# Optimization experiments

Hardware: AMD Instinct MI355X
Metric: run time of the kernel (lower is better)

The kernel has to match this reference:

```python
import jax, jax.numpy as jnp
import numpy as np

B, T, D, H = 64, 512, 512, 128

def swish(x):
    return x * jax.nn.sigmoid(x)

def setup_inputs() -> dict:
    key = jax.random.key(0)
    ks = jax.random.split(key, 8)
    X = jax.random.normal(ks[0], (B, T, D), dtype=jnp.float32)
    # strictly-upper-triangular random binary adjacency -> valid DAG
    adj = jax.random.bernoulli(ks[1], 0.3, (T, T)).astype(jnp.float32)
    dag = jnp.triu(adj, k=1)
    s = 1.0 / np.sqrt(D)
    Wk = jax.random.normal(ks[2], (H, D), dtype=jnp.float32) * s
    bk = jax.random.normal(ks[3], (H,), dtype=jnp.float32) * 0.01
    Wq = jax.random.normal(ks[4], (H, D), dtype=jnp.float32) * s
    bq = jax.random.normal(ks[5], (H,), dtype=jnp.float32) * 0.01
    Wv = jax.random.normal(ks[6], (H, D), dtype=jnp.float32) * s
    bv = jax.random.normal(ks[7], (H,), dtype=jnp.float32) * 0.01
    return {"X": X, "dag": dag, "Wk": Wk, "bk": bk, "Wq": Wq, "bq": bq, "Wv": Wv, "bv": bv}

def reference(X, dag, Wk, bk, Wq, bq, Wv, bv):
    K = swish(jnp.einsum('btd,hd->bth', X, Wk) + bk)  # [B,T,H]
    Q = swish(jnp.einsum('btd,hd->bth', X, Wq) + bq)
    V = swish(jnp.einsum('btd,hd->bth', X, Wv) + bv)
    S_qk = jnp.einsum('bqh,bkh->bqk', Q, K) / jnp.sqrt(jnp.float32(H))  # [B,T,T]
    dagT = dag.T  # [T,T]
    Sprime = dagT * jnp.einsum('ij,bjk->bik', dagT, S_qk)  # [B,T,T]
    # masked_fill(Sprime == 0, -inf) then softmax; rows that are all -inf
    # would produce NaN in torch and are replaced by zeros -> do it nan-free.
    nz = Sprime != 0
    masked = jnp.where(nz, Sprime, -jnp.inf)
    row_valid = jnp.any(nz, axis=-1, keepdims=True)  # [B,T,1]
    masked_safe = jnp.where(row_valid, masked, 0.0)
    probs = jax.nn.softmax(masked_safe, axis=-1) * row_valid  # [B,T,T]
    Vprime = jnp.einsum('ij,bjh->bih', dagT, V)  # [B,T,H]
    O = jnp.einsum('bqk,bkh->bqh', probs, V) + Vprime
    return O
```

## Files before the change

kernel.cpp:

```cpp
#include <hip/hip_runtime.h>
#include <hip/hip_bf16.h>

#define Bn 64
#define Tn 512
#define Dn 512
#define Hn 128
#define BT (Bn*Tn)

typedef unsigned short u16;
typedef unsigned long long u64;
typedef __attribute__((ext_vector_type(8))) short bf16x8;
typedef __attribute__((ext_vector_type(4))) float f32x4;

__device__ __forceinline__ u16 f2bf(float f) {
  union { float f; unsigned u; } v; v.f = f;
  unsigned r = (v.u + 0x7FFFu + ((v.u >> 16) & 1u)) >> 16;
  return (u16)r;
}

__device__ __forceinline__ bf16x8 pack8(float4 a, float4 b) {
  bf16x8 o;
  o[0] = (short)f2bf(a.x); o[1] = (short)f2bf(a.y);
  o[2] = (short)f2bf(a.z); o[3] = (short)f2bf(a.w);
  o[4] = (short)f2bf(b.x); o[5] = (short)f2bf(b.y);
  o[6] = (short)f2bf(b.z); o[7] = (short)f2bf(b.w);
  return o;
}

__device__ __forceinline__ void gload16(const void* g, void* lds) {
  __builtin_amdgcn_global_load_lds(
      (const __attribute__((address_space(1))) unsigned int*)g,
      (__attribute__((address_space(3))) unsigned int*)lds, 16, 0, 0);
}

__global__ __launch_bounds__(256) void conv_w3(const float4* __restrict__ Wk,
                                               const float4* __restrict__ Wq,
                                               const float4* __restrict__ Wv,
                                               ushort4* __restrict__ out) {
  int idx = blockIdx.x * 256 + threadIdx.x;
  int which = idx >> 14, j = idx & 16383;
  const float4* src = (which == 0) ? Wk : (which == 1) ? Wq : Wv;
  float4 v = src[j];
  ushort4 o; o.x = f2bf(v.x); o.y = f2bf(v.y); o.z = f2bf(v.z); o.w = f2bf(v.w);
  out[idx] = o;
}

__global__ __launch_bounds__(256) void dag_tr(const float* __restrict__ dag,
                                              u16* __restrict__ dagT,
                                              u64* __restrict__ bits) {
  __shared__ float s[64][65];
  int bx = blockIdx.x & 7, by = blockIdx.x >> 3;
  int r0 = by * 64, c0 = bx * 64;
  int t = threadIdx.x;
  int c4 = t & 15, rr = t >> 4;
#pragma unroll
  for (int q = 0; q < 4; ++q) {
    int r = rr + q * 16;
    float4 v = *(const float4*)&dag[(size_t)(r0 + r) * Tn + c0 + c4 * 4];
    s[c4 * 4 + 0][r] = v.x; s[c4 * 4 + 1][r] = v.y;
    s[c4 * 4 + 2][r] = v.z; s[c4 * 4 + 3][r] = v.w;
  }
  __syncthreads();
#pragma unroll
  for (int q = 0; q < 4; ++q) {
    int il = rr + q * 16;
    ushort4 o;
    u64 b4 = 0;
#pragma unroll
    for (int r = 0; r < 4; ++r) {
      float v = s[il][c4 * 4 + r];
      ((u16*)&o)[r] = f2bf(v);
      b4 |= (u64)(v != 0.f) << (c4 * 4 + r);
    }
    *(ushort4*)&dagT[(size_t)(c0 + il) * Tn + r0 + c4 * 4] = o;
    b4 |= __shfl_xor(b4, 1, 64);
    b4 |= __shfl_xor(b4, 2, 64);
    b4 |= __shfl_xor(b4, 4, 64);
    b4 |= __shfl_xor(b4, 8, 64);
    if (c4 == 0) bits[(size_t)(c0 + il) * 8 + (r0 >> 6)] = b4;
  }
}

__global__ __launch_bounds__(256, 2) void qkv3(
    const float* __restrict__ X, const u16* __restrict__ Wcat,
    const float* __restrict__ bk, const float* __restrict__ bq,
    const float* __restrict__ bv,
    u16* __restrict__ Kb, u16* __restrict__ QT, u16* __restrict__ VT) {
  __shared__ u16 sm[28672];
  int m0 = blockIdx.x * 64;
  int tid = threadIdx.x, lane = tid & 63, wave = tid >> 6;
  int col0 = lane & 15, rg = lane >> 4, kcb = rg * 16;
  int swl = (col0 & 7) << 4;
  int xrow = tid >> 2, xcq = tid & 3;
  f32x4 acc[3][4][2] = {};
  const char* Wb = (const char*)Wcat;
  char* smb = (char*)sm;

#define LOAD_X(kt_)                                                             \
  {                                                                             \
    const float4* s_ = (const float4*)(X + (size_t)(m0 + xrow) * Dn + (kt_) + xcq * 16); \
    xa0 = s_[0]; xa1 = s_[1]; xa2 = s_[2]; xa3 = s_[3];                         \
  }

  float4 xa0, xa1, xa2, xa3;
  LOAD_X(0);
  for (int kt = 0; kt < Dn; kt += 64) {
    {
      int sw = (xrow & 7) << 4;
      *(bf16x8*)(smb + xrow * 128 + ((xcq * 32) ^ sw)) = pack8(xa0, xa1);
      *(bf16x8*)(smb + xrow * 128 + ((xcq * 32 + 16) ^ sw)) = pack8(xa2, xa3);
    }
    if (kt + 64 < Dn) LOAD_X(kt + 64);
#pragma unroll
    for (int q = 0; q < 12; ++q) {
      int c2 = wave * 12 + q;
      int which = c2 >> 4, idx = c2 & 15;
      int flat = idx * 1024 + lane * 16;
      int row = flat >> 7, colb = flat & 127;
      int sw = (row & 7) << 4;
      gload16(Wb + (size_t)which * 131072 + (size_t)row * 1024 + (kt << 1) + (colb ^ sw),
              smb + 8192 + which * 16384 + idx * 1024);
    }
    __syncthreads();
    bf16x8 af[4][2];
#pragma unroll
    for (int m = 0; m < 4; ++m)
#pragma unroll
      for (int kk = 0; kk < 2; ++kk)
        af[m][kk] = *(const bf16x8*)(smb + (m * 16 + col0) * 128 + ((kk * 64 + kcb) ^ swl));
#pragma unroll
    for (int which = 0; which < 3; ++which) {
      bf16x8 bfr[2][2];
#pragma unroll
      for (int n = 0; n < 2; ++n)
#pragma unroll
        for (int kk = 0; kk < 2; ++kk)
          bfr[n][kk] = *(const bf16x8*)(smb + 8192 + which * 16384 +
                                        (wave * 32 + n * 16 + col0) * 128 + ((kk * 64 + kcb) ^ swl));
#pragma unroll
      for (int kk = 0; kk < 2; ++kk)
#pragma unroll
        for (int m = 0; m < 4; ++m)
#pragma unroll
          for (int n = 0; n < 2; ++n)
            acc[which][m][n] = __builtin_amdgcn_mfma_f32_16x16x32_bf16(
                af[m][kk], bfr[n][kk], acc[which][m][n], 0, 0, 0);
    }
    __syncthreads();
  }
#undef LOAD_X

  {
#pragma unroll
    for (int n = 0; n < 2; ++n) {
      int nl = wave * 32 + n * 16 + col0;
      float bs = bk[nl];
#pragma unroll
      for (int m = 0; m < 4; ++m)
#pragma unroll
        for (int r = 0; r < 4; ++r) {
          int tl = m * 16 + rg * 4 + r;
          float x = acc[0][m][n][r] + bs;
          *(u16*)(smb + tl * 256 + ((nl * 2) ^ ((tl & 7) << 4))) = f2bf(x / (1.f + __expf(-x)));
        }
    }
    __syncthreads();
#pragma unroll
    for (int p = 0; p < 4; ++p) {
      int c = p * 256 + tid;
      int t = c >> 4, c16 = c & 15;
      bf16x8 v = *(const bf16x8*)(smb + t * 256 + ((c16 * 16) ^ ((t & 7) << 4)));
      *(bf16x8*)&Kb[(size_t)(m0 + t) * Hn + c16 * 8] = v;
    }
  }
  int bb = m0 >> 9, tt0 = m0 & (Tn - 1);
#pragma unroll
  for (int which = 1; which < 3; ++which) {
    const float* bias = (which == 1) ? bq : bv;
    u16* dst = (which == 1) ? QT : VT;
    __syncthreads();
#pragma unroll
    for (int n = 0; n < 2; ++n) {
      int nl = wave * 32 + n * 16 + col0;
      float bs = bias[nl];
#pragma unroll
      for (int m = 0; m < 4; ++m)
#pragma unroll
        for (int r = 0; r < 4; ++r) {
          int tl = m * 16 + rg * 4 + r;
          float x = acc[which][m][n][r] + bs;
          *(u16*)(smb + nl * 128 + ((tl * 2) ^ ((nl & 7) << 4))) = f2bf(x / (1.f + __expf(-x)));
        }
    }
    __syncthreads();
#pragma unroll
    for (int p = 0; p < 4; ++p) {
      int c = p * 256 + tid;
      int h = c >> 3, c8 = c & 7;
      bf16x8 v = *(const bf16x8*)(smb + h * 128 + ((c8 * 16) ^ ((h & 7) << 4)));
      *(bf16x8*)&dst[((size_t)bb * Hn + h) * Tn + tt0 + c8 * 8] = v;
    }
  }
}

__global__ __launch_bounds__(256, 2) void dattn(
    const u16* __restrict__ dagT, const u16* __restrict__ QT,
    const u16* __restrict__ VT, const u16* __restrict__ Kb,
    const u64* __restrict__ dbits, float* __restrict__ O) {
  __shared__ char smA[65536];
  __shared__ u16 smQ2[8192];

  int bid = blockIdx.x;
  int xcd = bid & 7, rst = bid >> 3;
  int bx = rst & 7, b = (rst >> 3) * 8 + xcd;
  int m0 = bx * 64;
  int tid = threadIdx.x, lane = tid & 63, wave = tid >> 6;
  int col0 = lane & 15, g = lane >> 4;
  int swl = (col0 & 7) << 4;

  const char* Ab = (const char*)(dagT + (size_t)m0 * Tn);
  const char* Qb = (const char*)(QT + (size_t)b * Hn * Tn);
  const char* Vb = (const char*)(VT + (size_t)b * Hn * Tn);
  const char* Kb0 = (const char*)(Kb + (size_t)b * Tn * Hn);

  f32x4 accq[4][2] = {};
  for (int kt = 0; kt < Tn; kt += 64) {
#pragma unroll
    for (int q = 0; q < 2; ++q) {
      int ch = wave * 2 + q;
      int flat = ch * 1024 + lane * 16;
      int row = flat >> 7, colb = flat & 127;
      int sw = (row & 7) << 4;
      gload16(Ab + (size_t)row * 1024 + kt * 2 + (colb ^ sw), smA + ch * 1024);
    }
#pragma unroll
    for (int q = 0; q < 4; ++q) {
      int ch = wave * 4 + q;
      int flat = ch * 1024 + lane * 16;
      int row = flat >> 7, colb = flat & 127;
      int sw = (row & 7) << 4;
      gload16(Qb + (size_t)row * 1024 + kt * 2 + (colb ^ sw), smA + 8192 + ch * 1024);
    }
    __syncthreads();
    bf16x8 af[4][2], fq[2][2];
#pragma unroll
    for (int m = 0; m < 4; ++m)
#pragma unroll
      for (int kk = 0; kk < 2; ++kk)
        af[m][kk] = *(const bf16x8*)(smA + (m * 16 + col0) * 128 + ((kk * 64 + g * 16) ^ swl));
#pragma unroll
    for (int n = 0; n < 2; ++n)
#pragma unroll
      for (int kk = 0; kk < 2; ++kk)
        fq[n][kk] = *(const bf16x8*)(smA + 8192 + (wave * 32 + n * 16 + col0) * 128 + ((kk * 64 + g * 16) ^ swl));
#pragma unroll
    for (int kk = 0; kk < 2; ++kk)
#pragma unroll
      for (int m = 0; m < 4; ++m)
#pragma unroll
        for (int n = 0; n < 2; ++n)
          accq[m][n] = __builtin_amdgcn_mfma_f32_16x16x32_bf16(af[m][kk], fq[n][kk], accq[m][n], 0, 0, 0);
    __syncthreads();
  }

  const float scale = 0.08838834764831845f;
#pragma unroll
  for (int m = 0; m < 4; ++m)
#pragma unroll
    for (int n = 0; n < 2; ++n)
#pragma unroll
      for (int r = 0; r < 4; ++r) {
        int q = m * 16 + g * 4 + r;
        int h = wave * 32 + n * 16 + col0;
        *(u16*)((char*)smQ2 + q * 256 + ((h * 2) ^ ((q & 7) << 4))) = f2bf(accq[m][n][r] * scale);
      }

#define STAGE_K(c_, buf_)                                                      \
  {                                                                            \
    _Pragma("unroll")                                                          \
    for (int q = 0; q < 8; ++q) {                                              \
      int ch = wave * 8 + q;                                                   \
      int flat = ch * 1024 + lane * 16;                                        \
      int row = flat >> 8, colb = flat & 255;                                  \
      gload16(Kb0 + (size_t)((c_) * 128 + row) * 256 + (colb ^ ((row & 7) << 4)), \
              smA + (buf_) * 32768 + ch * 1024);                               \
    }                                                                          \
  }

  STAGE_K(0, 0);
  __syncthreads();

  int qrow = wave * 16 + col0;
  bf16x8 bq[4];
#pragma unroll
  for (int kk = 0; kk < 4; ++kk)
    bq[kk] = *(const bf16x8*)((char*)smQ2 + qrow * 256 + ((kk * 64 + g * 16) ^ ((qrow & 7) << 4)));
  const u64* dbq = dbits + (size_t)(m0 + qrow) * 8;
  u64 md[8];
#pragma unroll
  for (int w = 0; w < 8; ++w) md[w] = dbq[w];

  f32x4 sa[32] = {};
#pragma unroll
  for (int c = 0; c < 4; ++c) {
    if (c < 3) STAGE_K(c + 1, (c + 1) & 1);
    const char* kb = smA + (c & 1) * 32768;
#pragma unroll
    for (int t = 0; t < 8; ++t)
#pragma unroll
      for (int kk = 0; kk < 4; ++kk) {
        bf16x8 ak = *(const bf16x8*)(kb + (t * 16 + col0) * 256 + ((kk * 64 + g * 16) ^ swl));
        sa[c * 8 + t] = __builtin_amdgcn_mfma_f32_16x16x32_bf16(ak, bq[kk], sa[c * 8 + t], 0, 0, 0);
      }
    if (c < 3) __syncthreads();
  }

  float mx = -INFINITY;
#pragma unroll
  for (int t = 0; t < 32; ++t)
#pragma unroll
    for (int r = 0; r < 4; ++r) {
      int k = t * 16 + g * 4 + r;
      float v = ((md[k >> 6] >> (k & 63)) & 1) ? sa[t][r] : -INFINITY;
      sa[t][r] = v;
      mx = fmaxf(mx, v);
    }
  mx = fmaxf(mx, __shfl_xor(mx, 16, 64));
  mx = fmaxf(mx, __shfl_xor(mx, 32, 64));
  float mm = (mx == -INFINITY) ? 0.f : mx;

  float s = 0.f;
#pragma unroll
  for (int t = 0; t < 32; ++t)
#pragma unroll
    for (int r = 0; r < 4; ++r) {
      float v = sa[t][r];
      float e = (v == -INFINITY) ? 0.f : __expf(v - mm);
      sa[t][r] = e;
      s += e;
    }
  s += __shfl_xor(s, 16, 64);
  s += __shfl_xor(s, 32, 64);
  float inv = (s > 0.f) ? (1.f / s) : 0.f;

  ushort4 pk[32];
#pragma unroll
  for (int t = 0; t < 32; ++t) {
    ushort4 p;
#pragma unroll
    for (int r = 0; r < 4; ++r) {
      int k = t * 16 + g * 4 + r;
      float d = (float)((md[k >> 6] >> (k & 63)) & 1);
      ((u16*)&p)[r] = f2bf(sa[t][r] * inv + d);
    }
    pk[t] = p;
  }

  char* smP = smA;
  f32x4 acco[4][2] = {};
  int sww = (qrow & 7) << 4;

#pragma unroll
  for (int c = 0; c < 4; ++c) {
    __syncthreads();
#pragma unroll
    for (int tt = 0; tt < 8; ++tt)
      *(ushort4*)(smP + qrow * 256 + ((tt * 32 + g * 8) ^ sww)) = pk[c * 8 + tt];
    __syncthreads();

#pragma unroll
    for (int kk = 0; kk < 4; ++kk) {
      bf16x8 pa[4], vb[2];
#pragma unroll
      for (int m = 0; m < 4; ++m) {
        int row = m * 16 + col0;
        pa[m] = *(const bf16x8*)(smP + row * 256 + ((kk * 64 + g * 16) ^ ((row & 7) << 4)));
      }
#pragma unroll
      for (int n = 0; n < 2; ++n)
        vb[n] = *(const bf16x8*)(Vb + (size_t)(wave * 32 + n * 16 + col0) * 1024 + c * 256 + kk * 64 + g * 16);
#pragma unroll
      for (int m = 0; m < 4; ++m)
#pragma unroll
        for (int n = 0; n < 2; ++n)
          acco[m][n] = __builtin_amdgcn_mfma_f32_16x16x32_bf16(pa[m], vb[n], acco[m][n], 0, 0, 0);
    }
  }

#pragma unroll
  for (int m = 0; m < 4; ++m)
#pragma unroll
    for (int r = 0; r < 4; ++r) {
      int i = m0 + m * 16 + g * 4 + r;
#pragma unroll
      for (int n = 0; n < 2; ++n) {
        int h = wave * 32 + n * 16 + col0;
        O[((size_t)b * Tn + i) * Hn + h] = acco[m][n][r];
      }
    }
#undef STAGE_K
}

extern "C" void kernel_launch(void* const* d_in, const int* in_sizes, int n_in,
                              void* d_out, int out_size, void* d_ws, size_t ws_size,
                              hipStream_t stream) {
  const float* X   = (const float*)d_in[0];
  const float* dag = (const float*)d_in[1];
  const float* Wk  = (const float*)d_in[2];
  const float* bk  = (const float*)d_in[3];
  const float* Wq  = (const float*)d_in[4];
  const float* bq  = (const float*)d_in[5];
  const float* Wv  = (const float*)d_in[6];
  const float* bv  = (const float*)d_in[7];
  float* O = (float*)d_out;

  char* ws = (char*)d_ws;
  u16* Wcat = (u16*)(ws);
  u16* dagT = (u16*)(ws + 393216);
  u64* dbits= (u64*)(ws + 917504);
  u16* Kb   = (u16*)(ws + 950272);
  u16* QT   = (u16*)(ws + 9338880);
  u16* VT   = (u16*)(ws + 17727488);

  conv_w3<<<192, 256, 0, stream>>>((const float4*)Wk, (const float4*)Wq,
                                   (const float4*)Wv, (ushort4*)Wcat);
  dag_tr<<<64, 256, 0, stream>>>(dag, dagT, dbits);

  qkv3<<<BT / 64, 256, 0, stream>>>(X, Wcat, bk, bq, bv, Kb, QT, VT);
  dattn<<<512, 256, 0, stream>>>(dagT, QT, VT, Kb, dbits, O);
}
```

Measured before the change: 70.52 us.

## Merge prep kernels, remap qkv blocks per XCD, batch epilogue, double-buffer P

Merges the weight conversion and DAG transpose into one prep launch, dropping a kernel launch. The qkv3 block index is remapped so blocks of the same batch land on the same XCD, matching dattn's mapping for L2 locality. The K, Q and V epilogues now write to separate LDS regions in one pass, removing two barrier rounds. In dattn, the P tile is double-buffered so the next chunk's LDS write overlaps the current MFMA work, with one barrier per chunk instead of two. The cost is extra LDS usage and a larger, more complex epilogue.

```diff
diff --git a/kernel.cpp b/kernel.cpp
--- a/kernel.cpp
+++ b/kernel.cpp
@@ -33,51 +33,51 @@
       (__attribute__((address_space(3))) unsigned int*)lds, 16, 0, 0);
 }
 
-__global__ __launch_bounds__(256) void conv_w3(const float4* __restrict__ Wk,
-                                               const float4* __restrict__ Wq,
-                                               const float4* __restrict__ Wv,
-                                               ushort4* __restrict__ out) {
-  int idx = blockIdx.x * 256 + threadIdx.x;
-  int which = idx >> 14, j = idx & 16383;
-  const float4* src = (which == 0) ? Wk : (which == 1) ? Wq : Wv;
-  float4 v = src[j];
-  ushort4 o; o.x = f2bf(v.x); o.y = f2bf(v.y); o.z = f2bf(v.z); o.w = f2bf(v.w);
-  out[idx] = o;
-}
-
-__global__ __launch_bounds__(256) void dag_tr(const float* __restrict__ dag,
-                                              u16* __restrict__ dagT,
-                                              u64* __restrict__ bits) {
+__global__ __launch_bounds__(256) void prep(
+    const float4* __restrict__ Wk, const float4* __restrict__ Wq,
+    const float4* __restrict__ Wv, ushort4* __restrict__ Wcat,
+    const float* __restrict__ dag, u16* __restrict__ dagT,
+    u64* __restrict__ bits) {
   __shared__ float s[64][65];
-  int bx = blockIdx.x & 7, by = blockIdx.x >> 3;
-  int r0 = by * 64, c0 = bx * 64;
-  int t = threadIdx.x;
-  int c4 = t & 15, rr = t >> 4;
-#pragma unroll
-  for (int q = 0; q < 4; ++q) {
-    int r = rr + q * 16;
-    float4 v = *(const float4*)&dag[(size_t)(r0 + r) * Tn + c0 + c4 * 4];
-    s[c4 * 4 + 0][r] = v.x; s[c4 * 4 + 1][r] = v.y;
-    s[c4 * 4 + 2][r] = v.z; s[c4 * 4 + 3][r] = v.w;
-  }
-  __syncthreads();
-#pragma unroll
-  for (int q = 0; q < 4; ++q) {
-    int il = rr + q * 16;
-    ushort4 o;
-    u64 b4 = 0;
-#pragma unroll
-    for (int r = 0; r < 4; ++r) {
-      float v = s[il][c4 * 4 + r];
-      ((u16*)&o)[r] = f2bf(v);
-      b4 |= (u64)(v != 0.f) << (c4 * 4 + r);
-    }
-    *(ushort4*)&dagT[(size_t)(c0 + il) * Tn + r0 + c4 * 4] = o;
-    b4 |= __shfl_xor(b4, 1, 64);
-    b4 |= __shfl_xor(b4, 2, 64);
-    b4 |= __shfl_xor(b4, 4, 64);
-    b4 |= __shfl_xor(b4, 8, 64);
-    if (c4 == 0) bits[(size_t)(c0 + il) * 8 + (r0 >> 6)] = b4;
+  if (blockIdx.x < 192) {
+    int idx = blockIdx.x * 256 + threadIdx.x;
+    int which = idx >> 14, j = idx & 16383;
+    const float4* src = (which == 0) ? Wk : (which == 1) ? Wq : Wv;
+    float4 v = src[j];
+    ushort4 o; o.x = f2bf(v.x); o.y = f2bf(v.y); o.z = f2bf(v.z); o.w = f2bf(v.w);
+    Wcat[idx] = o;
+  } else {
+    int bid = blockIdx.x - 192;
+    int bx = bid & 7, by = bid >> 3;
+    int r0 = by * 64, c0 = bx * 64;
+    int t = threadIdx.x;
+    int c4 = t & 15, rr = t >> 4;
+#pragma unroll
+    for (int q = 0; q < 4; ++q) {
+      int r = rr + q * 16;
+      float4 v = *(const float4*)&dag[(size_t)(r0 + r) * Tn + c0 + c4 * 4];
+      s[c4 * 4 + 0][r] = v.x; s[c4 * 4 + 1][r] = v.y;
+      s[c4 * 4 + 2][r] = v.z; s[c4 * 4 + 3][r] = v.w;
+    }
+    __syncthreads();
+#pragma unroll
+    for (int q = 0; q < 4; ++q) {
+      int il = rr + q * 16;
+      ushort4 o;
+      u64 b4 = 0;
+#pragma unroll
+      for (int r = 0; r < 4; ++r) {
+        float v = s[il][c4 * 4 + r];
+        ((u16*)&o)[r] = f2bf(v);
+        b4 |= (u64)(v != 0.f) << (c4 * 4 + r);
+      }
+      *(ushort4*)&dagT[(size_t)(c0 + il) * Tn + r0 + c4 * 4] = o;
+      b4 |= __shfl_xor(b4, 1, 64);
+      b4 |= __shfl_xor(b4, 2, 64);
+      b4 |= __shfl_xor(b4, 4, 64);
+      b4 |= __shfl_xor(b4, 8, 64);
+      if (c4 == 0) bits[(size_t)(c0 + il) * 8 + (r0 >> 6)] = b4;
+    }
   }
 }
 
@@ -87,7 +87,11 @@
     const float* __restrict__ bv,
     u16* __restrict__ Kb, u16* __restrict__ QT, u16* __restrict__ VT) {
   __shared__ u16 sm[28672];
-  int m0 = blockIdx.x * 64;
+  int bid = blockIdx.x;
+  int xcd = bid & 7, idx = bid >> 3;
+  int b = (idx & 7) * 8 + xcd;
+  int rowblk = idx >> 3;
+  int m0 = b * Tn + rowblk * 64;
   int tid = threadIdx.x, lane = tid & 63, wave = tid >> 6;
   int col0 = lane & 15, rg = lane >> 4, kcb = rg * 16;
   int swl = (col0 & 7) << 4;
@@ -114,12 +118,12 @@
 #pragma unroll
     for (int q = 0; q < 12; ++q) {
       int c2 = wave * 12 + q;
-      int which = c2 >> 4, idx = c2 & 15;
-      int flat = idx * 1024 + lane * 16;
+      int which = c2 >> 4, widx = c2 & 15;
+      int flat = widx * 1024 + lane * 16;
       int row = flat >> 7, colb = flat & 127;
       int sw = (row & 7) << 4;
       gload16(Wb + (size_t)which * 131072 + (size_t)row * 1024 + (kt << 1) + (colb ^ sw),
-              smb + 8192 + which * 16384 + idx * 1024);
+              smb + 8192 + which * 16384 + widx * 1024);
     }
     __syncthreads();
     bf16x8 af[4][2];
@@ -154,51 +158,37 @@
 #pragma unroll
     for (int n = 0; n < 2; ++n) {
       int nl = wave * 32 + n * 16 + col0;
-      float bs = bk[nl];
+      float bsk = bk[nl], bsq = bq[nl], bsv = bv[nl];
 #pragma unroll
       for (int m = 0; m < 4; ++m)
 #pragma unroll
         for (int r = 0; r < 4; ++r) {
           int tl = m * 16 + rg * 4 + r;
-          float x = acc[0][m][n][r] + bs;
-          *(u16*)(smb + tl * 256 + ((nl * 2) ^ ((tl & 7) << 4))) = f2bf(x / (1.f + __expf(-x)));
+          float xk = acc[0][m][n][r] + bsk;
+          float xq = acc[1][m][n][r] + bsq;
+          float xv = acc[2][m][n][r] + bsv;
+          *(u16*)(smb + tl * 256 + ((nl * 2) ^ ((tl & 7) << 4))) = f2bf(xk / (1.f + __expf(-xk)));
+          *(u16*)(smb + 16384 + nl * 128 + ((tl * 2) ^ ((nl & 7) << 4))) = f2bf(xq / (1.f + __expf(-xq)));
+          *(u16*)(smb + 32768 + nl * 128 + ((tl * 2) ^ ((nl & 7) << 4))) = f2bf(xv / (1.f + __expf(-xv)));
         }
     }
     __syncthreads();
+    int tt0 = rowblk * 64;
 #pragma unroll
     for (int p = 0; p < 4; ++p) {
       int c = p * 256 + tid;
       int t = c >> 4, c16 = c & 15;
-      bf16x8 v = *(const bf16x8*)(smb + t * 256 + ((c16 * 16) ^ ((t & 7) << 4)));
-      *(bf16x8*)&Kb[(size_t)(m0 + t) * Hn + c16 * 8] = v;
-    }
-  }
-  int bb = m0 >> 9, tt0 = m0 & (Tn - 1);
-#pragma unroll
-  for (int which = 1; which < 3; ++which) {
-    const float* bias = (which == 1) ? bq : bv;
-    u16* dst = (which == 1) ? QT : VT;
-    __syncthreads();
-#pragma unroll
-    for (int n = 0; n < 2; ++n) {
-      int nl = wave * 32 + n * 16 + col0;
-      float bs = bias[nl];
-#pragma unroll
-      for (int m = 0; m < 4; ++m)
-#pragma unroll
-        for (int r = 0; r < 4; ++r) {
-          int tl = m * 16 + rg * 4 + r;
-          float x = acc[which][m][n][r] + bs;
-          *(u16*)(smb + nl * 128 + ((tl * 2) ^ ((nl & 7) << 4))) = f2bf(x / (1.f + __expf(-x)));
-        }
-    }
-    __syncthreads();
+      *(bf16x8*)&Kb[(size_t)(m0 + t) * Hn + c16 * 8] =
+          *(const bf16x8*)(smb + t * 256 + ((c16 * 16) ^ ((t & 7) << 4)));
+    }
 #pragma unroll
     for (int p = 0; p < 4; ++p) {
       int c = p * 256 + tid;
       int h = c >> 3, c8 = c & 7;
-      bf16x8 v = *(const bf16x8*)(smb + h * 128 + ((c8 * 16) ^ ((h & 7) << 4)));
-      *(bf16x8*)&dst[((size_t)bb * Hn + h) * Tn + tt0 + c8 * 8] = v;
+      *(bf16x8*)&QT[((size_t)b * Hn + h) * Tn + tt0 + c8 * 8] =
+          *(const bf16x8*)(smb + 16384 + h * 128 + ((c8 * 16) ^ ((h & 7) << 4)));
+      *(bf16x8*)&VT[((size_t)b * Hn + h) * Tn + tt0 + c8 * 8] =
+          *(const bf16x8*)(smb + 32768 + h * 128 + ((c8 * 16) ^ ((h & 7) << 4)));
     }
   }
 }
@@ -356,25 +346,29 @@
     pk[t] = p;
   }
 
-  char* smP = smA;
   f32x4 acco[4][2] = {};
   int sww = (qrow & 7) << 4;
 
+#define WRITE_P(c_, base_)                                                     \
+  {                                                                            \
+    _Pragma("unroll")                                                          \
+    for (int tt = 0; tt < 8; ++tt)                                             \
+      *(ushort4*)((base_) + qrow * 256 + ((tt * 32 + g * 8) ^ sww)) = pk[(c_) * 8 + tt]; \
+  }
+
+  WRITE_P(0, smA);
+  __syncthreads();
 #pragma unroll
   for (int c = 0; c < 4; ++c) {
-    __syncthreads();
-#pragma unroll
-    for (int tt = 0; tt < 8; ++tt)
-      *(ushort4*)(smP + qrow * 256 + ((tt * 32 + g * 8) ^ sww)) = pk[c * 8 + tt];
-    __syncthreads();
-
+    const char* pb = smA + (c & 1) * 16384;
+    if (c < 3) WRITE_P(c + 1, smA + ((c + 1) & 1) * 16384);
 #pragma unroll
     for (int kk = 0; kk < 4; ++kk) {
       bf16x8 pa[4], vb[2];
 #pragma unroll
       for (int m = 0; m < 4; ++m) {
         int row = m * 16 + col0;
-        pa[m] = *(const bf16x8*)(smP + row * 256 + ((kk * 64 + g * 16) ^ ((row & 7) << 4)));
+        pa[m] = *(const bf16x8*)(pb + row * 256 + ((kk * 64 + g * 16) ^ ((row & 7) << 4)));
       }
 #pragma unroll
       for (int n = 0; n < 2; ++n)
@@ -385,6 +379,7 @@
         for (int n = 0; n < 2; ++n)
           acco[m][n] = __builtin_amdgcn_mfma_f32_16x16x32_bf16(pa[m], vb[n], acco[m][n], 0, 0, 0);
     }
+    __syncthreads();
   }
 
 #pragma unroll
@@ -399,6 +394,7 @@
       }
     }
 #undef STAGE_K
+#undef WRITE_P
 }
 
 extern "C" void kernel_launch(void* const* d_in, const int* in_sizes, int n_in,
@@ -422,10 +418,8 @@
   u16* QT   = (u16*)(ws + 9338880);
   u16* VT   = (u16*)(ws + 17727488);
 
-  conv_w3<<<192, 256, 0, stream>>>((const float4*)Wk, (const float4*)Wq,
-                                   (const float4*)Wv, (ushort4*)Wcat);
-  dag_tr<<<64, 256, 0, stream>>>(dag, dagT, dbits);
-
+  prep<<<256, 256, 0, stream>>>((const float4*)Wk, (const float4*)Wq,
+                                (const float4*)Wv, (ushort4*)Wcat, dag, dagT, dbits);
   qkv3<<<BT / 64, 256, 0, stream>>>(X, Wcat, bk, bq, bv, Kb, QT, VT);
   dattn<<<512, 256, 0, stream>>>(dagT, QT, VT, Kb, dbits, O);
 }
```

After: 65.83 us. -6.6%, faster.
